# Kernel tuning notes

Measured on AMD Instinct MI355X. Metric: run time of the kernel, lower is better.

The kernel has to match this reference:

```python
import jax, jax.numpy as jnp
import numpy as np

N = 262144          # number of query points
NUM_AXES = 4        # input_dim + 2
RES = 512           # axis_resolution
EMB = 256           # embedding_dim
OUT = 3             # output_dim
W0 = 30.0           # Sine frequency


def setup_inputs() -> dict:
    key = jax.random.key(0)
    k_c, k_t, k_w1, k_b1, k_w2, k_b2 = jax.random.split(key, 6)
    coords = jax.random.uniform(k_c, (N, 2), jnp.float32, minval=-1.0, maxval=1.0)
    tables = jax.random.normal(k_t, (NUM_AXES, RES, EMB), jnp.float32) * 0.1
    # decoder: Linear(256,256) with first_layer_sine_init, Sine(30), Linear(256,3) with frequency_init(30)
    W1 = jax.random.uniform(k_w1, (256, EMB), jnp.float32, minval=-1.0 / EMB, maxval=1.0 / EMB)
    b1 = jax.random.uniform(k_b1, (256,), jnp.float32, minval=-0.0625, maxval=0.0625)
    lim2 = np.sqrt(6.0 / 256.0) / W0
    W2 = jax.random.uniform(k_w2, (OUT, 256), jnp.float32, minval=-lim2, maxval=lim2)
    b2 = jax.random.uniform(k_b2, (OUT,), jnp.float32, minval=-0.0625, maxval=0.0625)
    return {"coords": coords, "tables": tables, "W1": W1, "b1": b1, "W2": W2, "b2": b2}


def reference(coords, tables, W1, b1, W2, b2):
    # clamp input coords to [-1,1], build the 4 axis coordinates
    c = jnp.clip(coords, -1.0, 1.0)
    c = jnp.concatenate(
        [c, (c[:, 0:1] + c[:, 1:2]) * 0.5, (c[:, 0:1] - c[:, 1:2]) * 0.5], axis=-1
    )  # [N, 4]
    # linearInterpolate (vectorized over all axes at once)
    c = jnp.clip(c, -1.0, 0.999)
    t = (0.5 * c + 0.5) * (tables.shape[1] - 1)       # [N, 4] continuous index
    i0 = jnp.floor(t).astype(jnp.int32)               # [N, 4]
    w = (t - i0)[..., None]                           # [N, 4, 1]
    ax = jnp.arange(tables.shape[0])[None, :]         # [1, 4]
    v0 = tables[ax, i0]                               # [N, 4, EMB] gather
    v1 = tables[ax, i0 + 1]                           # [N, 4, EMB] gather
    emb = jnp.mean((1.0 - w) * v0 + w * v1, axis=1)   # [N, EMB] mean over axes
    # decoder: Linear -> Sine(30) -> Linear
    h = jnp.sin(W0 * (emb @ W1.T + b1))               # [N, 256]
    return h @ W2.T + b2                              # [N, 3]
```

## Files before the change

### kernel.cpp

```cpp
#include <hip/hip_runtime.h>
#include <hip/hip_fp16.h>

#define NPTS 262144
#define EMB  256
#define NROWS 2048

typedef _Float16 half_t;
typedef __attribute__((ext_vector_type(8))) _Float16 half8;
typedef __attribute__((ext_vector_type(2))) _Float16 half2v;

__global__ __launch_bounds__(256) void t2_precompute_kernel(
    const float* __restrict__ tables,
    const float* __restrict__ W1,
    half_t* __restrict__ T2)
{
    __shared__ __align__(16) float arow[8][EMB];
    const int row0 = blockIdx.x * 8;
    const int o = threadIdx.x;

    #pragma unroll
    for (int r = 0; r < 8; ++r)
        arow[r][o] = tables[(row0 + r) * EMB + o];
    __syncthreads();

    float acc[8] = {0.f, 0.f, 0.f, 0.f, 0.f, 0.f, 0.f, 0.f};
    const float4* __restrict__ w1v = reinterpret_cast<const float4*>(W1 + o * EMB);
    for (int ec = 0; ec < EMB / 4; ++ec) {
        const float4 w4 = w1v[ec];
        #pragma unroll
        for (int r = 0; r < 8; ++r) {
            const float4 a4 = *reinterpret_cast<const float4*>(&arow[r][ec * 4]);
            acc[r] = fmaf(w4.x, a4.x, acc[r]);
            acc[r] = fmaf(w4.y, a4.y, acc[r]);
            acc[r] = fmaf(w4.z, a4.z, acc[r]);
            acc[r] = fmaf(w4.w, a4.w, acc[r]);
        }
    }
    const float s = 7.5f * 0.15915494309189535f;
    #pragma unroll
    for (int r = 0; r < 8; ++r)
        T2[(row0 + r) * EMB + o] = (half_t)(s * acc[r]);
}

template <int CTRL>
__device__ __forceinline__ float dpp_add(float v) {
    const int vi = __builtin_bit_cast(int, v);
    const int sh = __builtin_amdgcn_update_dpp(0, vi, CTRL, 0xF, 0xF, true);
    return v + __builtin_bit_cast(float, sh);
}
__device__ __forceinline__ float reduce16(float v) {
    v = dpp_add<0xB1>(v);
    v = dpp_add<0x4E>(v);
    v = dpp_add<0x141>(v);
    v = dpp_add<0x140>(v);
    return v;
}

__global__ __launch_bounds__(256) void eval_kernel(
    const float* __restrict__ coords,
    const half_t* __restrict__ T2,
    const float* __restrict__ b1,
    const float* __restrict__ W2,
    const float* __restrict__ b2,
    float* __restrict__ out)
{
    const int lane = threadIdx.x & 63;
    const int g    = lane >> 4;
    const int l16  = lane & 15;
    const int dA   = l16 * 8;
    const int dB   = 128 + l16 * 8;

    const int wave   = blockIdx.x * 4 + (threadIdx.x >> 6);
    const int stride = gridDim.x * 4;

    const float sb = 30.f * 0.15915494309189535f;
    half8 biasA, biasB;
    #pragma unroll
    for (int i = 0; i < 8; ++i) {
        biasA[i] = (half_t)(sb * b1[dA + i]);
        biasB[i] = (half_t)(sb * b1[dB + i]);
    }
    half2v w2A[3][4], w2B[3][4];
    #pragma unroll
    for (int j = 0; j < 3; ++j)
        #pragma unroll
        for (int k = 0; k < 4; ++k) {
            w2A[j][k][0] = (half_t)W2[j * EMB + dA + 2 * k];
            w2A[j][k][1] = (half_t)W2[j * EMB + dA + 2 * k + 1];
            w2B[j][k][0] = (half_t)W2[j * EMB + dB + 2 * k];
            w2B[j][k][1] = (half_t)W2[j * EMB + dB + 2 * k + 1];
        }
    const float ob0 = b2[0], ob1 = b2[1], ob2 = b2[2];

    int Ca[4];
    #pragma unroll
    for (int a = 0; a < 4; ++a) Ca[a] = (a << 18) + (l16 << 4);

    const char* __restrict__ T2b = reinterpret_cast<const char*>(T2);
    const float TMAX = 0.9995f * 511.0f;

    auto calc = [&](int pq, int rb[4], half2v pw[4], int& pOut) {
        const int p = 4 * pq + g;
        pOut = p;
        const float2 cf = *reinterpret_cast<const float2*>(coords + 2 * p);
        const float txr = __builtin_amdgcn_fmed3f(fmaf(cf.x, 255.5f, 255.5f), 0.f, 511.f);
        const float tyr = __builtin_amdgcn_fmed3f(fmaf(cf.y, 255.5f, 255.5f), 0.f, 511.f);
        float t[4];
        t[0] = fminf(txr, TMAX);
        t[1] = fminf(tyr, TMAX);
        t[2] = fminf((txr + tyr) * 0.5f, TMAX);
        t[3] = fminf(fmaf(txr - tyr, 0.5f, 255.5f), TMAX);
        #pragma unroll
        for (int a = 0; a < 4; ++a) {
            const int i0 = (int)t[a];
            const float w = t[a] - (float)i0;
            rb[a] = (i0 << 9) + Ca[a];
            pw[a] = __builtin_bit_cast(half2v,
                        __builtin_amdgcn_cvt_pkrtz(1.f - w, w));
        }
    };
    auto loadA = [&](const int rb[4], half8 A0[4], half8 A1[4]) {
        #pragma unroll
        for (int a = 0; a < 4; ++a) {
            A0[a] = *reinterpret_cast<const half8*>(T2b + rb[a]);
            A1[a] = *reinterpret_cast<const half8*>(T2b + rb[a] + 512);
        }
    };
    auto loadB = [&](const int rb[4], half8 B0[4], half8 B1[4]) {
        #pragma unroll
        for (int a = 0; a < 4; ++a) {
            B0[a] = *reinterpret_cast<const half8*>(T2b + rb[a] + 256);
            B1[a] = *reinterpret_cast<const half8*>(T2b + rb[a] + 768);
        }
    };
    auto dots = [&](const half8& acc, const half2v (&w2)[3][4],
                    float& q0, float& q1, float& q2) {
        #pragma unroll
        for (int k = 0; k < 4; ++k) {
            const float s0 = __builtin_amdgcn_sinf((float)acc[2 * k]);
            const float s1 = __builtin_amdgcn_sinf((float)acc[2 * k + 1]);
            const half2v hp = __builtin_bit_cast(half2v,
                                  __builtin_amdgcn_cvt_pkrtz(s0, s1));
            q0 = __builtin_amdgcn_fdot2(hp, w2[0][k], q0, false);
            q1 = __builtin_amdgcn_fdot2(hp, w2[1][k], q1, false);
            q2 = __builtin_amdgcn_fdot2(hp, w2[2][k], q2, false);
        }
    };

    int    rbC[4]; half2v pwC[4]; int pC;
    int    rbN[4]; half2v pwN[4]; int pN = 0;
    half8  A0[4], A1[4], B0[4], B1[4];

    calc(wave, rbC, pwC, pC);
    loadA(rbC, A0, A1);
    loadB(rbC, B0, B1);

    #pragma unroll
    for (int k = 0; k < 4; ++k) {
        if (k < 3) calc(wave + (k + 1) * stride, rbN, pwN, pN);

        half8 accA = biasA;
        #pragma unroll
        for (int a = 0; a < 4; ++a) {
            accA = A0[a] * pwC[a][0] + accA;
            accA = A1[a] * pwC[a][1] + accA;
        }
        if (k < 3) loadA(rbN, A0, A1);

        float q0 = 0.f, q1 = 0.f, q2 = 0.f;
        dots(accA, w2A, q0, q1, q2);

        half8 accB = biasB;
        #pragma unroll
        for (int a = 0; a < 4; ++a) {
            accB = B0[a] * pwC[a][0] + accB;
            accB = B1[a] * pwC[a][1] + accB;
        }
        if (k < 3) loadB(rbN, B0, B1);

        dots(accB, w2B, q0, q1, q2);

        q0 = reduce16(q0);
        q1 = reduce16(q1);
        q2 = reduce16(q2);

        if (l16 == 0) {
            *reinterpret_cast<float3*>(out + 3 * pC) =
                make_float3(q0 + ob0, q1 + ob1, q2 + ob2);
        }

        #pragma unroll
        for (int a = 0; a < 4; ++a) { rbC[a] = rbN[a]; pwC[a] = pwN[a]; }
        pC = pN;
    }
}

extern "C" void kernel_launch(void* const* d_in, const int* in_sizes, int n_in,
                              void* d_out, int out_size, void* d_ws, size_t ws_size,
                              hipStream_t stream) {
    const float* coords = (const float*)d_in[0];
    const float* tables = (const float*)d_in[1];
    const float* W1     = (const float*)d_in[2];
    const float* b1     = (const float*)d_in[3];
    const float* W2     = (const float*)d_in[4];
    const float* b2     = (const float*)d_in[5];
    float* out = (float*)d_out;

    half_t* T2 = (half_t*)d_ws;

    hipLaunchKernelGGL(t2_precompute_kernel, dim3(NROWS / 8), dim3(256), 0, stream,
                       tables, W1, T2);
    hipLaunchKernelGGL(eval_kernel, dim3(4096), dim3(256), 0, stream,
                       coords, T2, b1, W2, b2, out);
}
```

Before: 58.37 us.

## Drop manual software pipelining in eval kernel and raise occupancy bound

Removes the explicit double-buffered prefetch of the next point's table rows and computes, loads, and reduces each point in a simple unrolled loop. It also asks for 8 waves per SIMD through launch_bounds. The aim is to cut register pressure from holding two sets of 16 half8 buffers, and to rely on higher occupancy to hide gather latency in place of in-thread prefetch. The risk is exposed load latency if the compiler does not reorder loads across iterations, or spills under the tighter register cap.

```diff
diff --git a/kernel.cpp b/kernel.cpp
--- a/kernel.cpp
+++ b/kernel.cpp
@@ -56,7 +56,7 @@
     return v;
 }
 
-__global__ __launch_bounds__(256) void eval_kernel(
+__global__ __launch_bounds__(256, 8) void eval_kernel(
     const float* __restrict__ coords,
     const half_t* __restrict__ T2,
     const float* __restrict__ b1,
@@ -99,9 +99,9 @@
     const char* __restrict__ T2b = reinterpret_cast<const char*>(T2);
     const float TMAX = 0.9995f * 511.0f;
 
-    auto calc = [&](int pq, int rb[4], half2v pw[4], int& pOut) {
-        const int p = 4 * pq + g;
-        pOut = p;
+    #pragma unroll
+    for (int k = 0; k < 4; ++k) {
+        const int p = 4 * (wave + k * stride) + g;
         const float2 cf = *reinterpret_cast<const float2*>(coords + 2 * p);
         const float txr = __builtin_amdgcn_fmed3f(fmaf(cf.x, 255.5f, 255.5f), 0.f, 511.f);
         const float tyr = __builtin_amdgcn_fmed3f(fmaf(cf.y, 255.5f, 255.5f), 0.f, 511.f);
@@ -110,6 +110,9 @@
         t[1] = fminf(tyr, TMAX);
         t[2] = fminf((txr + tyr) * 0.5f, TMAX);
         t[3] = fminf(fmaf(txr - tyr, 0.5f, 255.5f), TMAX);
+
+        int rb[4];
+        half2v pw[4];
         #pragma unroll
         for (int a = 0; a < 4; ++a) {
             const int i0 = (int)t[a];
@@ -118,80 +121,56 @@
             pw[a] = __builtin_bit_cast(half2v,
                         __builtin_amdgcn_cvt_pkrtz(1.f - w, w));
         }
-    };
-    auto loadA = [&](const int rb[4], half8 A0[4], half8 A1[4]) {
+
+        half8 A0[4], A1[4], B0[4], B1[4];
         #pragma unroll
         for (int a = 0; a < 4; ++a) {
-            A0[a] = *reinterpret_cast<const half8*>(T2b + rb[a]);
-            A1[a] = *reinterpret_cast<const half8*>(T2b + rb[a] + 512);
+            const char* base = T2b + rb[a];
+            A0[a] = *reinterpret_cast<const half8*>(base);
+            B0[a] = *reinterpret_cast<const half8*>(base + 256);
+            A1[a] = *reinterpret_cast<const half8*>(base + 512);
+            B1[a] = *reinterpret_cast<const half8*>(base + 768);
         }
-    };
-    auto loadB = [&](const int rb[4], half8 B0[4], half8 B1[4]) {
+
+        half8 accA = biasA, accB = biasB;
         #pragma unroll
         for (int a = 0; a < 4; ++a) {
-            B0[a] = *reinterpret_cast<const half8*>(T2b + rb[a] + 256);
-            B1[a] = *reinterpret_cast<const half8*>(T2b + rb[a] + 768);
+            accA = A0[a] * pw[a][0] + accA;
+            accA = A1[a] * pw[a][1] + accA;
+            accB = B0[a] * pw[a][0] + accB;
+            accB = B1[a] * pw[a][1] + accB;
         }
-    };
-    auto dots = [&](const half8& acc, const half2v (&w2)[3][4],
-                    float& q0, float& q1, float& q2) {
+
+        float q0 = 0.f, q1 = 0.f, q2 = 0.f;
         #pragma unroll
-        for (int k = 0; k < 4; ++k) {
-            const float s0 = __builtin_amdgcn_sinf((float)acc[2 * k]);
-            const float s1 = __builtin_amdgcn_sinf((float)acc[2 * k + 1]);
+        for (int kk = 0; kk < 4; ++kk) {
+            const float s0 = __builtin_amdgcn_sinf((float)accA[2 * kk]);
+            const float s1 = __builtin_amdgcn_sinf((float)accA[2 * kk + 1]);
             const half2v hp = __builtin_bit_cast(half2v,
                                   __builtin_amdgcn_cvt_pkrtz(s0, s1));
-            q0 = __builtin_amdgcn_fdot2(hp, w2[0][k], q0, false);
-            q1 = __builtin_amdgcn_fdot2(hp, w2[1][k], q1, false);
-            q2 = __builtin_amdgcn_fdot2(hp, w2[2][k], q2, false);
+            q0 = __builtin_amdgcn_fdot2(hp, w2A[0][kk], q0, false);
+            q1 = __builtin_amdgcn_fdot2(hp, w2A[1][kk], q1, false);
+            q2 = __builtin_amdgcn_fdot2(hp, w2A[2][kk], q2, false);
         }
-    };
-
-    int    rbC[4]; half2v pwC[4]; int pC;
-    int    rbN[4]; half2v pwN[4]; int pN = 0;
-    half8  A0[4], A1[4], B0[4], B1[4];
-
-    calc(wave, rbC, pwC, pC);
-    loadA(rbC, A0, A1);
-    loadB(rbC, B0, B1);
-
-    #pragma unroll
-    for (int k = 0; k < 4; ++k) {
-        if (k < 3) calc(wave + (k + 1) * stride, rbN, pwN, pN);
-
-        half8 accA = biasA;
         #pragma unroll
-        for (int a = 0; a < 4; ++a) {
-            accA = A0[a] * pwC[a][0] + accA;
-            accA = A1[a] * pwC[a][1] + accA;
+        for (int kk = 0; kk < 4; ++kk) {
+            const float s0 = __builtin_amdgcn_sinf((float)accB[2 * kk]);
+            const float s1 = __builtin_amdgcn_sinf((float)accB[2 * kk + 1]);
+            const half2v hp = __builtin_bit_cast(half2v,
+                                  __builtin_amdgcn_cvt_pkrtz(s0, s1));
+            q0 = __builtin_amdgcn_fdot2(hp, w2B[0][kk], q0, false);
+            q1 = __builtin_amdgcn_fdot2(hp, w2B[1][kk], q1, false);
+            q2 = __builtin_amdgcn_fdot2(hp, w2B[2][kk], q2, false);
         }
-        if (k < 3) loadA(rbN, A0, A1);
-
-        float q0 = 0.f, q1 = 0.f, q2 = 0.f;
-        dots(accA, w2A, q0, q1, q2);
-
-        half8 accB = biasB;
-        #pragma unroll
-        for (int a = 0; a < 4; ++a) {
-            accB = B0[a] * pwC[a][0] + accB;
-            accB = B1[a] * pwC[a][1] + accB;
-        }
-        if (k < 3) loadB(rbN, B0, B1);
-
-        dots(accB, w2B, q0, q1, q2);
 
         q0 = reduce16(q0);
         q1 = reduce16(q1);
         q2 = reduce16(q2);
 
         if (l16 == 0) {
-            *reinterpret_cast<float3*>(out + 3 * pC) =
+            *reinterpret_cast<float3*>(out + 3 * p) =
                 make_float3(q0 + ob0, q1 + ob1, q2 + ob2);
         }
-
-        #pragma unroll
-        for (int a = 0; a < 4; ++a) { rbC[a] = rbN[a]; pwC[a] = pwN[a]; }
-        pC = pN;
     }
 }
 
```

After: 67.55 us. 1.16x slower.
